# Performance work log

Hardware: AMD Instinct MI355X
Metric: run time of the kernel (lower is better)

## Reference

```python
import jax, jax.numpy as jnp
import numpy as np
from jax import lax

B, C, H, W = 16, 256, 64, 64
NUM_OPS = 4   # identity, conv3x3, conv5x5, avgpool3x3
TOPK = 2
TEMP = 1.0
EPS = 1e-6


def _conv(x, w, b, pad):
    # x: [B,C,H,W], w: [O,I,k,k] -> [B,O,H,W]
    y = lax.conv_general_dilated(x, w, (1, 1), [(pad, pad), (pad, pad)],
                                 dimension_numbers=("NCHW", "OIHW", "NCHW"))
    return y + b[None, :, None, None]


def _avgpool3(x):
    # AvgPool2d(3, stride=1, padding=1, count_include_pad=True)
    s = lax.reduce_window(x, 0.0, lax.add, (1, 1, 3, 3), (1, 1, 1, 1),
                          [(0, 0), (0, 0), (1, 1), (1, 1)])
    return s / 9.0


def setup_inputs() -> dict:
    key = jax.random.key(0)
    ks = jax.random.split(key, 9)
    sc_in = 1.0 / np.sqrt(C)
    return {
        "x": jax.random.normal(ks[0], (B, C, H, W), jnp.float32),
        # global router: Conv2d(C, NUM_OPS, 1) applied after global avg pool
        "gr_w": jax.random.normal(ks[1], (NUM_OPS, C, 1, 1), jnp.float32) * sc_in,
        "gr_b": jnp.zeros((NUM_OPS,), jnp.float32),
        # spatial router: Conv2d(C, NUM_OPS, 1)
        "sr_w": jax.random.normal(ks[2], (NUM_OPS, C, 1, 1), jnp.float32) * sc_in,
        "sr_b": jnp.zeros((NUM_OPS,), jnp.float32),
        # operator pool convs (channel-preserving, 'same' padding)
        "conv3_w": jax.random.normal(ks[3], (C, C, 3, 3), jnp.float32) * (1.0 / np.sqrt(C * 9)),
        "conv3_b": jnp.zeros((C,), jnp.float32),
        "conv5_w": jax.random.normal(ks[4], (C, C, 5, 5), jnp.float32) * (1.0 / np.sqrt(C * 25)),
        "conv5_b": jnp.zeros((C,), jnp.float32),
    }


def reference(x, gr_w, gr_b, sr_w, sr_b, conv3_w, conv3_b, conv5_w, conv5_b):
    # --- routing logits ---
    g = jnp.mean(x, axis=(2, 3))                               # [B,C]  (AdaptiveAvgPool2d(1))
    g = jnp.einsum("bc,oc->bo", g, gr_w[:, :, 0, 0]) + gr_b    # [B,O]  (1x1 conv)
    s = jnp.einsum("bchw,oc->bohw", x, sr_w[:, :, 0, 0]) + sr_b[None, :, None, None]
    logits = (g[:, :, None, None] + s) / max(TEMP, 1e-6)       # [B,O,H,W]
    weights = jax.nn.softmax(logits, axis=1)

    # --- per-pixel top-k masking + renormalization ---
    wt = jnp.moveaxis(weights, 1, -1)                          # [B,H,W,O]
    _, idx = lax.top_k(wt, TOPK)                               # [B,H,W,K]
    mask = jax.nn.one_hot(idx, NUM_OPS, dtype=wt.dtype).sum(-2)  # [B,H,W,O]
    wm = wt * mask
    wm = wm / (wm.sum(-1, keepdims=True) + EPS)
    w = jnp.moveaxis(wm, -1, 1)                                # [B,O,H,W]

    # --- weighted mixture of operators ---
    out = (x * w[:, 0:1]
           + _conv(x, conv3_w, conv3_b, 1) * w[:, 1:2]
           + _conv(x, conv5_w, conv5_b, 2) * w[:, 2:3]
           + _avgpool3(x) * w[:, 3:4])
    return out
```

## Files before the change

### kernel.cpp

```cpp
#include <hip/hip_runtime.h>
#include <hip/hip_bf16.h>

#define B_ 16
#define C_ 256
#define H_ 64
#define W_ 64
#define HW_ 4096

typedef __attribute__((ext_vector_type(4))) float f32x4;
typedef __attribute__((ext_vector_type(8))) short short8;

__device__ short g_zero[2048];

__device__ __forceinline__ short bf16_of(float f) {
    union { float f; unsigned u; } v; v.f = f;
    unsigned r = v.u + 0x7fffu + ((v.u >> 16) & 1u);
    return (short)(r >> 16);
}

__device__ __forceinline__ void gload16(const void* g, void* l) {
    __builtin_amdgcn_global_load_lds(
        (const __attribute__((address_space(1))) void*)g,
        (__attribute__((address_space(3))) void*)l, 16, 0, 0);
}

__global__ void prep_w_k(const float* __restrict__ w3, const float* __restrict__ w5,
                         short* __restrict__ W3f, short* __restrict__ W5f) {
    int idx = blockIdx.x * 256 + threadIdx.x;
    const int n5 = 25 * 65536;
    if (idx < n5) {
        int j = idx & 7, lane = (idx >> 3) & 63, kstep = (idx >> 9) & 7,
            otile = (idx >> 12) & 15, tap = idx >> 16;
        int o = otile * 16 + (lane & 15);
        int c = kstep * 32 + ((lane >> 4) << 3) + j;
        int ky = tap / 5, kx = tap % 5;
        W5f[idx] = bf16_of(w5[((o * C_ + c) * 5 + ky) * 5 + kx]);
    } else {
        int i2 = idx - n5;
        if (i2 < 9 * 65536) {
            int j = i2 & 7, lane = (i2 >> 3) & 63, kstep = (i2 >> 9) & 7,
                otile = (i2 >> 12) & 15, tap = i2 >> 16;
            int o = otile * 16 + (lane & 15);
            int c = kstep * 32 + ((lane >> 4) << 3) + j;
            int ky = tap / 3, kx = tap % 3;
            W3f[i2] = bf16_of(w3[((o * C_ + c) * 3 + ky) * 3 + kx]);
        }
    }
}

__global__ void transpose_k(const float* __restrict__ x, short* __restrict__ Xt) {
    __shared__ float tile[64][65];
    int bid = blockIdx.x;
    int cblk = bid & 3, pblk = (bid >> 2) & 63, b = bid >> 8;
    int t = threadIdx.x;
    const float* xb = x + (size_t)(b * C_ + cblk * 64) * HW_ + pblk * 64;
    int px = t & 63, c4 = t >> 6;
    #pragma unroll
    for (int it = 0; it < 16; ++it) {
        int ci = c4 + it * 4;
        tile[ci][px] = xb[(size_t)ci * HW_ + px];
    }
    __syncthreads();
    short* xtb = Xt + (size_t)(b * HW_ + pblk * 64) * C_ + cblk * 64;
    int c8 = (t & 7) * 8, pw0 = t >> 3;
    #pragma unroll
    for (int it = 0; it < 2; ++it) {
        int pw = pw0 + it * 32;
        short8 v;
        #pragma unroll
        for (int k = 0; k < 8; ++k) v[k] = bf16_of(tile[c8 + k][pw]);
        *(short8*)(xtb + (size_t)pw * C_ + c8) = v;
    }
}

__global__ void gpool_k(const float* __restrict__ x, double* __restrict__ gp) {
    __shared__ double red[256];
    int bc = blockIdx.x;
    const float* p = x + (size_t)bc * HW_;
    double s = 0.0;
    for (int i = threadIdx.x; i < HW_; i += 256) s += (double)p[i];
    red[threadIdx.x] = s;
    __syncthreads();
    for (int st = 128; st > 0; st >>= 1) {
        if (threadIdx.x < st) red[threadIdx.x] += red[threadIdx.x + st];
        __syncthreads();
    }
    if (threadIdx.x == 0) gp[bc] = red[0];
}

__global__ void gvec_k(const double* __restrict__ gp, const float* __restrict__ grw,
                       const float* __restrict__ grb, double* __restrict__ g) {
    int b = blockIdx.x;
    int o = threadIdx.x >> 6, lane = threadIdx.x & 63;
    double s = 0.0;
    for (int c = lane; c < C_; c += 64)
        s += gp[b * C_ + c] * (double)grw[o * C_ + c];
    #pragma unroll
    for (int off = 32; off > 0; off >>= 1) s += __shfl_down(s, off);
    if (lane == 0) g[b * 4 + o] = s * (1.0 / 4096.0) + (double)grb[o];
}

__global__ void routing_k(const float* __restrict__ x, const float* __restrict__ srw,
                          const float* __restrict__ srb, const double* __restrict__ g,
                          float* __restrict__ w4) {
    __shared__ double red[4][64][4];
    int t = threadIdx.x;
    int pl = t & 63, part = t >> 6;
    int p = blockIdx.x * 64 + pl;
    int b = p >> 12, pix = p & 4095;
    const float* xb = x + (size_t)b * C_ * HW_ + pix;
    double s[4] = {0, 0, 0, 0};
    for (int c = part * 64; c < part * 64 + 64; ++c) {
        double xv = (double)xb[(size_t)c * HW_];
        #pragma unroll
        for (int o = 0; o < 4; ++o) s[o] += xv * (double)srw[o * C_ + c];
    }
    #pragma unroll
    for (int o = 0; o < 4; ++o) red[part][pl][o] = s[o];
    __syncthreads();
    if (part == 0) {
        double l[4];
        #pragma unroll
        for (int o = 0; o < 4; ++o)
            l[o] = red[0][pl][o] + red[1][pl][o] + red[2][pl][o] + red[3][pl][o]
                   + (double)srb[o] + g[b * 4 + o];
        double m = fmax(fmax(l[0], l[1]), fmax(l[2], l[3]));
        double e[4], sum = 0.0;
        #pragma unroll
        for (int o = 0; o < 4; ++o) { e[o] = exp(l[o] - m); sum += e[o]; }
        double wv[4];
        #pragma unroll
        for (int o = 0; o < 4; ++o) wv[o] = e[o] / sum;
        int i1 = 0;
        for (int o = 1; o < 4; ++o) if (wv[o] > wv[i1]) i1 = o;
        int i2 = (i1 == 0) ? 1 : 0;
        for (int o = 0; o < 4; ++o) { if (o == i1) continue; if (wv[o] > wv[i2]) i2 = o; }
        double sc = 1.0 / (wv[i1] + wv[i2] + 1e-6);
        #pragma unroll
        for (int o = 0; o < 4; ++o) {
            float r = (o == i1 || o == i2) ? (float)(wv[o] * sc) : 0.0f;
            w4[((size_t)b * 4 + o) * HW_ + pix] = r;
        }
    }
}

__launch_bounds__(256, 3)
__global__ void conv_fused_k(const short* __restrict__ Xt, const short* __restrict__ W5f,
                             const short* __restrict__ W3f, const float* __restrict__ x,
                             const float* __restrict__ w4, const float* __restrict__ b3,
                             const float* __restrict__ b5, float* __restrict__ out) {
    __shared__ __align__(16) char lds[5 * 68 * 128];
    int swz = ((blockIdx.x & 7) << 8) | (blockIdx.x >> 3);
    int h = swz & 63, nb = (swz >> 6) & 1, b = swz >> 7;
    int t = threadIdx.x;
    int wv = t >> 6, lane = t & 63;
    int l15 = lane & 15, l4 = lane >> 4;

    f32x4 acc5[4][2], acc3[4][2];
    #pragma unroll
    for (int mi = 0; mi < 4; ++mi)
        #pragma unroll
        for (int ni = 0; ni < 2; ++ni) {
            acc5[mi][ni] = (f32x4){0.f, 0.f, 0.f, 0.f};
            acc3[mi][ni] = (f32x4){0.f, 0.f, 0.f, 0.f};
        }

    if (t < 160) {
        int part = t & 7, ci = (t >> 3) & 3, row = t >> 5;
        int col = (ci < 2) ? ci : (64 + ci);
        *(short8*)(lds + (row * 68 + col) * 128 + part * 16) = (short8){0,0,0,0,0,0,0,0};
    }

    const size_t xt_b = (size_t)b * HW_ * C_;
    const short* zp = g_zero;

    const int wvu = __builtin_amdgcn_readfirstlane(wv);
    const int otile0 = nb * 8 + wvu * 2;
    const short* W5l = W5f + (size_t)lane * 8;
    const short* W3l = W3f + (size_t)lane * 8;

    for (int chunk = 0; chunk < 4; ++chunk) {
        int c0 = chunk * 64;
        __syncthreads();
        #pragma unroll
        for (int it = 0; it < 10; ++it) {
            int idx = t + it * 256;
            int part = idx & 7;
            int ci   = (idx >> 3) & 7;
            int g8   = (idx >> 6) & 7;
            int row  = idx >> 9;
            int col  = 2 + g8 * 8 + ci;
            int gr = h + row - 2, gc = g8 * 8 + ci;
            int p = part ^ (col & 7);
            const short* src = ((unsigned)gr < 64u)
                ? Xt + xt_b + (size_t)(gr * 64 + gc) * 256 + c0 + p * 8
                : zp + ((idx & 63) << 3);
            gload16(src, lds + (row * 68 + 2 + g8 * 8) * 128);
        }
        __syncthreads();

        const int kst0 = chunk * 2, kst1 = chunk * 2 + 1;
        short8 av[4], b5X[2], b5Y[2], b3X[2], b3Y[2];

        #pragma unroll
        for (int ni = 0; ni < 2; ++ni)
            b5X[ni] = *(const short8*)(W5l +
                (size_t)(((otile0 + ni) * 8 + kst0)) * 512);

        int dy = -2, dx = -2;
        for (int tap = 0; tap < 25; ++tap) {
            const bool inner = (dy >= -1 && dy <= 1 && dx >= -1 && dx <= 1);
            const int tap3 = (dy + 1) * 3 + (dx + 1);
            const int ndx = (dx == 2) ? -2 : dx + 1;
            const int ndy = (dx == 2) ? dy + 1 : dy;

            #pragma unroll
            for (int mi = 0; mi < 4; ++mi) {
                int col_s = mi * 16 + l15 + dx + 2;
                int kb = l4 * 16;
                av[mi] = *(const short8*)(lds + ((dy + 2) * 68 + col_s) * 128
                                           + (kb ^ ((col_s & 7) << 4)));
            }
            #pragma unroll
            for (int ni = 0; ni < 2; ++ni)
                b5Y[ni] = *(const short8*)(W5l +
                    (size_t)((tap * 16 + otile0 + ni) * 8 + kst1) * 512);
            if (inner) {
                #pragma unroll
                for (int ni = 0; ni < 2; ++ni)
                    b3Y[ni] = *(const short8*)(W3l +
                        (size_t)((tap3 * 16 + otile0 + ni) * 8 + kst1) * 512);
            }
            __builtin_amdgcn_s_setprio(1);
            #pragma unroll
            for (int ni = 0; ni < 2; ++ni)
                #pragma unroll
                for (int mi = 0; mi < 4; ++mi)
                    acc5[mi][ni] = __builtin_amdgcn_mfma_f32_16x16x32_bf16(
                        av[mi], b5X[ni], acc5[mi][ni], 0, 0, 0);
            if (inner) {
                #pragma unroll
                for (int ni = 0; ni < 2; ++ni)
                    #pragma unroll
                    for (int mi = 0; mi < 4; ++mi)
                        acc3[mi][ni] = __builtin_amdgcn_mfma_f32_16x16x32_bf16(
                            av[mi], b3X[ni], acc3[mi][ni], 0, 0, 0);
            }
            __builtin_amdgcn_s_setprio(0);

            #pragma unroll
            for (int mi = 0; mi < 4; ++mi) {
                int col_s = mi * 16 + l15 + dx + 2;
                int kb = l4 * 16 + 64;
                av[mi] = *(const short8*)(lds + ((dy + 2) * 68 + col_s) * 128
                                           + (kb ^ ((col_s & 7) << 4)));
            }
            if (tap < 24) {
                const bool innern = (ndy >= -1 && ndy <= 1 && ndx >= -1 && ndx <= 1);
                const int tap3n = (ndy + 1) * 3 + (ndx + 1);
                #pragma unroll
                for (int ni = 0; ni < 2; ++ni)
                    b5X[ni] = *(const short8*)(W5l +
                        (size_t)(((tap + 1) * 16 + otile0 + ni) * 8 + kst0) * 512);
                if (innern) {
                    #pragma unroll
                    for (int ni = 0; ni < 2; ++ni)
                        b3X[ni] = *(const short8*)(W3l +
                            (size_t)((tap3n * 16 + otile0 + ni) * 8 + kst0) * 512);
                }
            }
            __builtin_amdgcn_s_setprio(1);
            #pragma unroll
            for (int ni = 0; ni < 2; ++ni)
                #pragma unroll
                for (int mi = 0; mi < 4; ++mi)
                    acc5[mi][ni] = __builtin_amdgcn_mfma_f32_16x16x32_bf16(
                        av[mi], b5Y[ni], acc5[mi][ni], 0, 0, 0);
            if (inner) {
                #pragma unroll
                for (int ni = 0; ni < 2; ++ni)
                    #pragma unroll
                    for (int mi = 0; mi < 4; ++mi)
                        acc3[mi][ni] = __builtin_amdgcn_mfma_f32_16x16x32_bf16(
                            av[mi], b3Y[ni], acc3[mi][ni], 0, 0, 0);
            }
            __builtin_amdgcn_s_setprio(0);

            dy = ndy; dx = ndx;
        }
    }

    __syncthreads();
    float* colsum = (float*)lds;
    float* w4row = colsum + 128 * 65;
    for (int idx = t; idx < 128 * 64; idx += 256) {
        int ch = idx >> 6, px = idx & 63;
        const float* xp = x + (size_t)(b * C_ + nb * 128 + ch) * HW_ + px;
        float s = xp[h * 64];
        if (h > 0) s += xp[(h - 1) * 64];
        if (h < 63) s += xp[(h + 1) * 64];
        colsum[ch * 65 + px] = s;
    }
    {
        int o = t >> 6, px = t & 63;
        w4row[o * 64 + px] = w4[((size_t)b * 4 + o) * HW_ + h * 64 + px];
    }
    __syncthreads();

    #pragma unroll
    for (int ni = 0; ni < 2; ++ni) {
        int ch_l = wvu * 32 + ni * 16 + l15;
        int ch = nb * 128 + ch_l;
        float b3v = b3[ch], b5v = b5[ch];
        const size_t orow = ((size_t)(b * C_ + ch) * H_ + h) * W_;
        #pragma unroll
        for (int mi = 0; mi < 4; ++mi) {
            int px0 = mi * 16 + l4 * 4;
            f32x4 res;
            #pragma unroll
            for (int rr = 0; rr < 4; ++rr) {
                int px = px0 + rr;
                float c3 = acc3[mi][ni][rr] + b3v;
                float c5 = acc5[mi][ni][rr] + b5v;
                float cs = colsum[ch_l * 65 + px];
                float csl = (px > 0) ? colsum[ch_l * 65 + px - 1] : 0.f;
                float csr = (px < 63) ? colsum[ch_l * 65 + px + 1] : 0.f;
                float ap = (cs + csl + csr) * (1.0f / 9.0f);
                float xv = x[orow + px];
                float w0 = w4row[px], w1 = w4row[64 + px], w2 = w4row[128 + px],
                      w3v = w4row[192 + px];
                res[rr] = w0 * xv + w1 * c3 + w2 * c5 + w3v * ap;
            }
            *(f32x4*)(out + orow + px0) = res;
        }
    }
}

extern "C" void kernel_launch(void* const* d_in, const int* in_sizes, int n_in,
                              void* d_out, int out_size, void* d_ws, size_t ws_size,
                              hipStream_t stream) {
    const float* x   = (const float*)d_in[0];
    const float* grw = (const float*)d_in[1];
    const float* grb = (const float*)d_in[2];
    const float* srw = (const float*)d_in[3];
    const float* srb = (const float*)d_in[4];
    const float* c3w = (const float*)d_in[5];
    const float* c3b = (const float*)d_in[6];
    const float* c5w = (const float*)d_in[7];
    const float* c5b = (const float*)d_in[8];
    float* out = (float*)d_out;
    char* ws = (char*)d_ws;

    short*  Xt  = (short*)(ws);
    short*  W5f = (short*)(ws + 33554432);
    short*  W3f = (short*)(ws + 36831232);
    float*  w4  = (float*)(ws + 38010880);
    double* gp  = (double*)(ws + 39059456);
    double* g   = (double*)(ws + 39092224);

    prep_w_k   <<<8704, 256, 0, stream>>>(c3w, c5w, W3f, W5f);
    transpose_k<<<4096, 256, 0, stream>>>(x, Xt);
    gpool_k    <<<4096, 256, 0, stream>>>(x, gp);
    gvec_k     <<<16,   256, 0, stream>>>(gp, grw, grb, g);
    routing_k  <<<1024, 256, 0, stream>>>(x, srw, srb, g, w4);
    conv_fused_k<<<2048, 256, 0, stream>>>(Xt, W5f, W3f, x, w4, c3b, c5b, out);
}
```

Baseline: 349.6 us.

## Fuse global pooling and spatial router dot into the transpose kernel

```diff
diff --git a/kernel.cpp b/kernel.cpp
--- a/kernel.cpp
+++ b/kernel.cpp
@@ -73,6 +73,54 @@
     }
 }
 
+__global__ void transpose_fused_k(const float* __restrict__ x,
+                                  const float* __restrict__ srw,
+                                  short* __restrict__ Xt,
+                                  double* __restrict__ gp_part,
+                                  double* __restrict__ s_part) {
+    __shared__ float tile[64][65];
+    __shared__ double psum[4][64];
+    int bid = blockIdx.x;
+    int cblk = bid & 3, pblk = (bid >> 2) & 63, b = bid >> 8;
+    int t = threadIdx.x;
+    const float* xb = x + (size_t)(b * C_ + cblk * 64) * HW_ + pblk * 64;
+    int px = t & 63, c4 = t >> 6;
+    #pragma unroll
+    for (int it = 0; it < 16; ++it) {
+        int ci = c4 + it * 4;
+        tile[ci][px] = xb[(size_t)ci * HW_ + px];
+    }
+    __syncthreads();
+    short* xtb = Xt + (size_t)(b * HW_ + pblk * 64) * C_ + cblk * 64;
+    int c8 = (t & 7) * 8, pw0 = t >> 3;
+    #pragma unroll
+    for (int it = 0; it < 2; ++it) {
+        int pw = pw0 + it * 32;
+        short8 v;
+        #pragma unroll
+        for (int k = 0; k < 8; ++k) v[k] = bf16_of(tile[c8 + k][pw]);
+        *(short8*)(xtb + (size_t)pw * C_ + c8) = v;
+    }
+    {
+        int ch = t & 63, qt = t >> 6;
+        double s = 0.0;
+        #pragma unroll
+        for (int k = 0; k < 16; ++k) s += (double)tile[ch][qt * 16 + k];
+        psum[qt][ch] = s;
+    }
+    {
+        int o = t >> 6;
+        double sp = 0.0;
+        for (int ch = 0; ch < 64; ++ch)
+            sp += (double)tile[ch][px] * (double)srw[o * C_ + cblk * 64 + ch];
+        s_part[(size_t)bid * 256 + o * 64 + px] = sp;
+    }
+    __syncthreads();
+    if (t < 64)
+        gp_part[(size_t)bid * 64 + t] =
+            ((psum[0][t] + psum[1][t]) + psum[2][t]) + psum[3][t];
+}
+
 __global__ void gpool_k(const float* __restrict__ x, double* __restrict__ gp) {
     __shared__ double red[256];
     int bc = blockIdx.x;
@@ -98,6 +146,25 @@
     #pragma unroll
     for (int off = 32; off > 0; off >>= 1) s += __shfl_down(s, off);
     if (lane == 0) g[b * 4 + o] = s * (1.0 / 4096.0) + (double)grb[o];
+}
+
+__global__ void gvec2_k(const double* __restrict__ gp_part,
+                        const float* __restrict__ grw,
+                        const float* __restrict__ grb, double* __restrict__ g) {
+    __shared__ double red[256];
+    int b = blockIdx.x, t = threadIdx.x;
+    int cblk = t >> 6, ch = t & 63;
+    double s = 0.0;
+    for (int pblk = 0; pblk < 64; ++pblk)
+        s += gp_part[((size_t)(b * 256 + pblk * 4 + cblk) << 6) + ch];
+    red[t] = s;
+    __syncthreads();
+    int o = t >> 6, lane = t & 63;
+    double s2 = 0.0;
+    for (int c = lane; c < C_; c += 64) s2 += red[c] * (double)grw[o * C_ + c];
+    #pragma unroll
+    for (int off = 32; off > 0; off >>= 1) s2 += __shfl_down(s2, off);
+    if (lane == 0) g[b * 4 + o] = s2 * (1.0 / 4096.0) + (double)grb[o];
 }
 
 __global__ void routing_k(const float* __restrict__ x, const float* __restrict__ srw,
@@ -141,6 +208,40 @@
             float r = (o == i1 || o == i2) ? (float)(wv[o] * sc) : 0.0f;
             w4[((size_t)b * 4 + o) * HW_ + pix] = r;
         }
+    }
+}
+
+__global__ void routing_sm_k(const double* __restrict__ s_part,
+                             const float* __restrict__ srb,
+                             const double* __restrict__ g,
+                             float* __restrict__ w4) {
+    int p = blockIdx.x * 256 + threadIdx.x;
+    int b = p >> 12, pix = p & 4095;
+    int pblk = pix >> 6, px = pix & 63;
+    double l[4];
+    #pragma unroll
+    for (int o = 0; o < 4; ++o) {
+        const size_t base = (size_t)(b * 256 + pblk * 4) * 256 + o * 64 + px;
+        l[o] = ((s_part[base] + s_part[base + 256]) + s_part[base + 512])
+               + s_part[base + 768];
+        l[o] = l[o] + (double)srb[o] + g[b * 4 + o];
+    }
+    double m = fmax(fmax(l[0], l[1]), fmax(l[2], l[3]));
+    double e[4], sum = 0.0;
+    #pragma unroll
+    for (int o = 0; o < 4; ++o) { e[o] = exp(l[o] - m); sum += e[o]; }
+    double wv[4];
+    #pragma unroll
+    for (int o = 0; o < 4; ++o) wv[o] = e[o] / sum;
+    int i1 = 0;
+    for (int o = 1; o < 4; ++o) if (wv[o] > wv[i1]) i1 = o;
+    int i2 = (i1 == 0) ? 1 : 0;
+    for (int o = 0; o < 4; ++o) { if (o == i1) continue; if (wv[o] > wv[i2]) i2 = o; }
+    double sc = 1.0 / (wv[i1] + wv[i2] + 1e-6);
+    #pragma unroll
+    for (int o = 0; o < 4; ++o) {
+        float r = (o == i1 || o == i2) ? (float)(wv[o] * sc) : 0.0f;
+        w4[((size_t)b * 4 + o) * HW_ + pix] = r;
     }
 }
 
@@ -355,13 +456,23 @@
     short*  W5f = (short*)(ws + 33554432);
     short*  W3f = (short*)(ws + 36831232);
     float*  w4  = (float*)(ws + 38010880);
-    double* gp  = (double*)(ws + 39059456);
-    double* g   = (double*)(ws + 39092224);
-
-    prep_w_k   <<<8704, 256, 0, stream>>>(c3w, c5w, W3f, W5f);
-    transpose_k<<<4096, 256, 0, stream>>>(x, Xt);
-    gpool_k    <<<4096, 256, 0, stream>>>(x, gp);
-    gvec_k     <<<16,   256, 0, stream>>>(gp, grw, grb, g);
-    routing_k  <<<1024, 256, 0, stream>>>(x, srw, srb, g, w4);
+    double* g   = (double*)(ws + 39059456);
+    double* gp_part = (double*)(ws + 39059968);
+    double* s_part  = (double*)(ws + 41157120);
+    double* gp = gp_part;
+
+    const bool fused = (ws_size >= 49545728ull);
+
+    prep_w_k<<<8704, 256, 0, stream>>>(c3w, c5w, W3f, W5f);
+    if (fused) {
+        transpose_fused_k<<<4096, 256, 0, stream>>>(x, srw, Xt, gp_part, s_part);
+        gvec2_k   <<<16,  256, 0, stream>>>(gp_part, grw, grb, g);
+        routing_sm_k<<<256, 256, 0, stream>>>(s_part, srb, g, w4);
+    } else {
+        transpose_k<<<4096, 256, 0, stream>>>(x, Xt);
+        gpool_k    <<<4096, 256, 0, stream>>>(x, gp);
+        gvec_k     <<<16,   256, 0, stream>>>(gp, grw, grb, g);
+        routing_k  <<<1024, 256, 0, stream>>>(x, srw, srb, g, w4);
+    }
     conv_fused_k<<<2048, 256, 0, stream>>>(Xt, W5f, W3f, x, w4, c3b, c5b, out);
 }
```

Result: faster. 318.3 us (-8.9%).
